# Kernel optimization log

Hardware: AMD Instinct MI355X
Metric: run time of the kernel (lower is better)

Reference implementation:

```python
import jax, jax.numpy as jnp
import numpy as np

H = 512  # hidden_dim
DIN = 64  # input_dim
DOUT = 1  # output_dim
B, T = 256, 512


def _lstm_layer(x_seq, W_ih, W_hh, b_ih, b_hh):
    """x_seq: [T, B, D_in]; returns full hidden sequence [T, B, H].
    PyTorch gate order along the 4H axis: i, f, g, o."""
    x_proj = jnp.einsum('tbd,gd->tbg', x_seq, W_ih) + b_ih + b_hh  # [T,B,4H]

    def cell(carry, xg):
        h, c = carry
        gates = xg + h @ W_hh.T  # [B,4H]
        i, f, g, o = jnp.split(gates, 4, axis=-1)
        c = jax.nn.sigmoid(f) * c + jax.nn.sigmoid(i) * jnp.tanh(g)
        h = jax.nn.sigmoid(o) * jnp.tanh(c)
        return (h, c), h

    h0 = jnp.zeros((x_seq.shape[1], H), x_seq.dtype)
    c0 = jnp.zeros_like(h0)
    _, hs = jax.lax.scan(cell, (h0, c0), x_proj)
    return hs


def setup_inputs() -> dict:
    key = jax.random.key(0)
    ks = jax.random.split(key, 11)
    s = 1.0 / np.sqrt(H)  # PyTorch LSTM init scale
    u = lambda k, shp: jax.random.uniform(k, shp, jnp.float32, -s, s)
    return {
        'x': jax.random.normal(ks[0], (B, T, DIN), jnp.float32),
        'W_ih0': u(ks[1], (4 * H, DIN)),
        'W_hh0': u(ks[2], (4 * H, H)),
        'b_ih0': u(ks[3], (4 * H,)),
        'b_hh0': u(ks[4], (4 * H,)),
        'W_ih1': u(ks[5], (4 * H, H)),
        'W_hh1': u(ks[6], (4 * H, H)),
        'b_ih1': u(ks[7], (4 * H,)),
        'b_hh1': u(ks[8], (4 * H,)),
        'fc_W': u(ks[9], (DOUT, H)),
        'fc_b': u(ks[10], (DOUT,)),
    }


def reference(x, W_ih0, W_hh0, b_ih0, b_hh0, W_ih1, W_hh1, b_ih1, b_hh1, fc_W, fc_b):
    xs = jnp.swapaxes(x, 0, 1)  # [T,B,DIN] time-major for scan
    h1 = _lstm_layer(xs, W_ih0, W_hh0, b_ih0, b_hh0)  # [T,B,H]
    h2 = _lstm_layer(h1, W_ih1, W_hh1, b_ih1, b_hh1)  # [T,B,H]
    last = h2[-1]  # [B,H] == out[:, -1, :]
    return last @ fc_W.T + fc_b  # [B,DOUT]
```

## Files before the change

kernel.cpp:

```cpp
#include <hip/hip_runtime.h>


typedef _Float16 f16;
typedef _Float16 f16x8 __attribute__((ext_vector_type(8)));
typedef float    f32x4 __attribute__((ext_vector_type(4)));

constexpr int NB   = 256;
constexpr int NT   = 512;
constexpr int NH   = 512;
constexpr int NDIN = 64;

constexpr int L0_KC = 18;
constexpr int L1_KC = 32;
constexpr int L0_IMG_HALVES = 4 * L0_KC * 64 * 8;
constexpr int L1_IMG_HALVES = 4 * L1_KC * 64 * 8;

constexpr int RING = 16;
constexpr int SLOT_F16 = 131072;

constexpr size_t BAR_OFF   = 0;
constexpr size_t AUX_OFF   = 16384;
constexpr size_t BIAS0_OFF = 20480;
constexpr size_t BIAS1_OFF = 28672;
constexpr size_t FLAG_OFF  = 36864;
constexpr size_t H0R_OFF   = 131072;
constexpr size_t H1R_OFF   = H0R_OFF + (size_t)RING * SLOT_F16 * 2;
constexpr size_t W0I_OFF   = H1R_OFF + (size_t)RING * SLOT_F16 * 2;
constexpr size_t W1I_OFF   = W0I_OFF + 2359296;
constexpr size_t WS_NEED   = W1I_OFF + 4194304;

constexpr int LDS_STAGE = 131072;
constexpr int LDS_GO    = 139264;
constexpr int LDS_SIZE  = 139520;

constexpr int WDOG = 1 << 20;

__global__ void prep_weights(const float* __restrict__ Wih0, const float* __restrict__ Whh0,
                             const float* __restrict__ Wih1, const float* __restrict__ Whh1,
                             char* __restrict__ ws) {
    int idx = blockIdx.x * 256 + threadIdx.x;
    const int L0_CH = 32 * 4 * L0_KC * 64;
    const int L1_CH = 32 * 4 * L1_KC * 64;
    if (idx < L0_CH) {
        int lam = idx & 63;
        int kc  = (idx >> 6) % L0_KC;
        int nf  = ((idx >> 6) / L0_KC) & 3;
        int ht  = idx / (64 * L0_KC * 4);
        int g   = nf * NH + ht * 16 + (lam & 15);
        int kb  = kc * 32 + (lam >> 4) * 8;
        f16x8 v;
#pragma unroll
        for (int j = 0; j < 8; ++j) {
            int k = kb + j;
            float val = (k < NDIN) ? Wih0[(size_t)g * NDIN + k]
                                   : Whh0[(size_t)g * NH + (k - NDIN)];
            v[j] = (f16)val;
        }
        f16* dst = (f16*)(ws + W0I_OFF) + (size_t)ht * L0_IMG_HALVES
                 + ((size_t)(nf * L0_KC + kc) * 64 + lam) * 8;
        *(f16x8*)dst = v;
    } else if (idx < L0_CH + L1_CH) {
        int i2  = idx - L0_CH;
        int lam = i2 & 63;
        int kc  = (i2 >> 6) % L1_KC;
        int nf  = ((i2 >> 6) / L1_KC) & 3;
        int ht  = i2 / (64 * L1_KC * 4);
        int g   = nf * NH + ht * 16 + (lam & 15);
        int kb  = kc * 32 + (lam >> 4) * 8;
        f16x8 v;
#pragma unroll
        for (int j = 0; j < 8; ++j) {
            int k = kb + j;
            float val = (k < NH) ? Wih1[(size_t)g * NH + k]
                                 : Whh1[(size_t)g * NH + (k - NH)];
            v[j] = (f16)val;
        }
        f16* dst = (f16*)(ws + W1I_OFF) + (size_t)ht * L1_IMG_HALVES
                 + ((size_t)(nf * L1_KC + kc) * 64 + lam) * 8;
        *(f16x8*)dst = v;
    }
}

__global__ void prep_state(const float* __restrict__ bih0, const float* __restrict__ bhh0,
                           const float* __restrict__ bih1, const float* __restrict__ bhh1,
                           char* __restrict__ ws) {
    int idx    = blockIdx.x * 256 + threadIdx.x;
    int stride = gridDim.x * 256;
    if (idx < 2048) {
        ((float*)(ws + BIAS0_OFF))[idx] = bih0[idx] + bhh0[idx];
    } else if (idx < 4096) {
        int i = idx - 2048;
        ((float*)(ws + BIAS1_OFF))[i] = bih1[i] + bhh1[i];
    }
    uint4 z; z.x = z.y = z.z = z.w = 0u;
    for (int i = idx; i < 1280; i += stride)
        ((uint4*)(ws + BAR_OFF))[i] = z;
    for (int i = idx; i < 2048; i += stride)
        ((uint4*)(ws + FLAG_OFF))[i] = z;
    const int RINGU4 = (int)((size_t)2 * RING * SLOT_F16 * 2 / 16);
    for (int i = idx; i < RINGU4; i += stride)
        ((uint4*)(ws + H0R_OFF))[i] = z;
}

__device__ __forceinline__ float sigf(float x) { return 1.f / (1.f + __expf(-x)); }
__device__ __forceinline__ float tanhx(float x) { float e = __expf(2.f * x); return 1.f - 2.f / (e + 1.f); }

__device__ __forceinline__ void st8_sys(unsigned long long* p, unsigned long long v) {
    __hip_atomic_store(p, v, __ATOMIC_RELAXED, __HIP_MEMORY_SCOPE_SYSTEM);
}

template <int SLP>
__device__ __forceinline__ void spin_cnt(unsigned* p, unsigned tgt) {
    int it = 0;
    while (__hip_atomic_fetch_add(p, 0u, __ATOMIC_RELAXED, __HIP_MEMORY_SCOPE_AGENT) < tgt) {
        __builtin_amdgcn_s_sleep(SLP);
        if (++it > WDOG) break;
    }
}

#define MFMA16(a, b, c) __builtin_amdgcn_mfma_f32_16x16x32_f16((a), (b), (c), 0, 0, 0)

__global__ __launch_bounds__(320, 1) void lstm_persist(char* __restrict__ ws,
                                                       const float* __restrict__ xin,
                                                       const float* __restrict__ fcW,
                                                       const float* __restrict__ fcb,
                                                       float* __restrict__ out) {
    extern __shared__ __align__(16) char smem[];
    f16*      sW     = (f16*)smem;
    f16*      hstage = (f16*)(smem + LDS_STAGE);
    unsigned* go     = (unsigned*)(smem + LDS_GO);

    const int tid  = threadIdx.x;
    const int lam  = tid & 63;
    const int w    = tid >> 6;
    const int col  = lam & 15;
    const int quad = lam >> 4;

    const int bid   = blockIdx.x;
    const int gid   = bid & 7;
    const int layer = gid >> 2;
    const int b0    = (gid & 3) * 64;
    const int ht    = bid >> 3;
    const int h0c   = ht * 16;
    const int KCx   = layer ? L1_KC : L0_KC;

    auto cntp = [&](int g, int slot) -> unsigned* {
        return (unsigned*)(ws + BAR_OFF + (size_t)(slot * 8 + g) * 128);
    };
    unsigned* flags = (unsigned*)(ws + FLAG_OFF);
    unsigned* hsk   = (unsigned*)(ws + AUX_OFF);
    unsigned* trdy  = (unsigned*)(ws + AUX_OFF + 128);
    unsigned* modep = (unsigned*)(ws + AUX_OFF + 256);
    unsigned* finp  = (unsigned*)(ws + AUX_OFF + 384);
    unsigned* tpat  = (unsigned*)(ws + AUX_OFF + 1024);
    unsigned* gvote = (unsigned*)(ws + AUX_OFF + 2048);

    if (tid == 0) {
        go[0] = 0u; go[1] = 0u;
        __hip_atomic_store(flags + (size_t)bid * 32 + 2, 0x5EED0000u + (unsigned)bid,
                           __ATOMIC_RELAXED, __HIP_MEMORY_SCOPE_AGENT);
        __hip_atomic_fetch_add(hsk, 1u, __ATOMIC_RELEASE, __HIP_MEMORY_SCOPE_AGENT);
        {
            int it = 0;
            while (__hip_atomic_fetch_add(hsk, 0u, __ATOMIC_RELAXED, __HIP_MEMORY_SCOPE_AGENT) < 256u) {
                __builtin_amdgcn_s_sleep(8);
                if (++it > WDOG) break;
            }
        }
        if (bid == 0) {
            for (int i = 0; i < 16; ++i)
                __hip_atomic_store(tpat + i * 16, 0xC0FFEE00u + (unsigned)i,
                                   __ATOMIC_RELAXED, __HIP_MEMORY_SCOPE_SYSTEM);
            asm volatile("s_waitcnt vmcnt(0)" ::: "memory");
            __hip_atomic_fetch_add(trdy, 1u, __ATOMIC_RELAXED, __HIP_MEMORY_SCOPE_AGENT);
        }
        if (bid == 1) {
            int it = 0;
            while (__hip_atomic_fetch_add(trdy, 0u, __ATOMIC_RELAXED, __HIP_MEMORY_SCOPE_AGENT) < 1u) {
                __builtin_amdgcn_s_sleep(8);
                if (++it > WDOG) break;
            }
            unsigned ok = 1u;
            for (int i = 0; i < 16; ++i)
                if (__hip_atomic_load(tpat + i * 16, __ATOMIC_RELAXED, __HIP_MEMORY_SCOPE_SYSTEM)
                    != 0xC0FFEE00u + (unsigned)i) ok = 0u;
            __hip_atomic_fetch_add(modep, 2u | (ok ? 0u : 1u), __ATOMIC_RELAXED, __HIP_MEMORY_SCOPE_AGENT);
        }
        unsigned mv; int spins = 0;
        while ((mv = __hip_atomic_fetch_add(modep, 0u, __ATOMIC_RELAXED, __HIP_MEMORY_SCOPE_AGENT)) < 2u) {
            __builtin_amdgcn_s_sleep(16);
            if (++spins > (1 << 22)) { mv = 3u; break; }
        }
        ((unsigned*)hstage)[1] = mv & 1u;
    }
    __syncthreads();
    const unsigned needRel = ((unsigned*)hstage)[1];
    __syncthreads();

    if (tid < 64) {
        unsigned seen = (lam < 32) ? 0u : 1u;
        unsigned expv = 0x5EED0000u + (unsigned)(lam * 8 + gid);
        int it = 0, done_at = 1 << 30;
        for (;;) {
            if (!seen && lam < 32) {
                unsigned v = __hip_atomic_load(flags + (size_t)(lam * 8 + gid) * 32 + 2,
                                               __ATOMIC_RELAXED, __HIP_MEMORY_SCOPE_AGENT);
                if (v == expv) seen = 1u;
            }
            ++it;
            if (__all((int)seen)) { done_at = it; break; }
            if (it >= 64) break;
        }
        unsigned ok = (done_at <= 12) ? 1u : 0u;
        if (lam == 0)
            __hip_atomic_fetch_add(gvote + (size_t)gid * 32, 0x10000u | ok,
                                   __ATOMIC_RELAXED, __HIP_MEMORY_SCOPE_AGENT);
    }
    __syncthreads();
    if (tid == 0) {
        unsigned gv = 0u; int sp2 = 0;
        for (;;) {
            gv = __hip_atomic_fetch_add(gvote + (size_t)gid * 32, 0u,
                                        __ATOMIC_RELAXED, __HIP_MEMORY_SCOPE_AGENT);
            if ((gv >> 16) >= 32u) break;
            __builtin_amdgcn_s_sleep(8);
            if (++sp2 > (1 << 20)) { gv = 0u; break; }
        }
        ((unsigned*)hstage)[0] = (((gv >> 16) >= 32u) && ((gv & 0xFFFFu) == 32u)) ? 1u : 0u;
    }
    __syncthreads();
    const unsigned fastgrp = ((unsigned*)hstage)[0];
    unsigned       fastE1  = fastgrp;
    __syncthreads();

    f16* h0ring = (f16*)(ws + H0R_OFF);
    f16* h1ring = (f16*)(ws + H1R_OFF);
    const float* bias = (const float*)(ws + (layer ? BIAS1_OFF : BIAS0_OFF));
    const f16*   wimg = (const f16*)(ws + (layer ? W1I_OFF : W0I_OFF))
                      + (size_t)ht * (layer ? L1_IMG_HALVES : L0_IMG_HALVES);

    {
        const int n16 = KCx * 4 * 64;
        const uint4* src = (const uint4*)wimg;
        uint4* dst = (uint4*)sW;
        for (int i = tid; i < n16; i += 320) dst[i] = src[i];
    }
    __syncthreads();

    const float bi_i = bias[0 * NH + h0c + col];
    const float bi_f = bias[1 * NH + h0c + col];
    const float bi_g = bias[2 * NH + h0c + col];
    const float bi_o = bias[3 * NH + h0c + col];

    float cst[4];
#pragma unroll
    for (int r = 0; r < 4; ++r) cst[r] = 0.f;

    const f16x8* sBf = (const f16x8*)sW;
    const int rA   = b0 + (w & 3) * 16 + col;
    const int rofs = rA * 16 + (quad & 1) * 8;
    const int hq   = (quad >> 1) * 4096;

    unsigned long long pr0 = 0, pr1 = 0, pr2 = 0, pr3 = 0;
    unsigned useRmw = 0u;
    unsigned vflag  = 0u;

    if (w == 4 && lam == 0) {
        if (layer == 1) spin_cnt<4>(cntp(gid - 4, 0), 32u);
        __hip_atomic_store(&go[0], 1u, __ATOMIC_RELAXED, __HIP_MEMORY_SCOPE_WORKGROUP);
    }

    for (int s = 0; s < NT; ++s) {
        const unsigned us = (unsigned)s;

        f32x4 ai = {0.f,0.f,0.f,0.f}, af = {0.f,0.f,0.f,0.f};
        f32x4 ag = {0.f,0.f,0.f,0.f}, ao = {0.f,0.f,0.f,0.f};

        if (w == 4) {
            if (!fastgrp) {
                if (s > 0) {
                    if (fastE1) {
                        int it = 0;
                        for (;;) {
                            unsigned v = 0xFFFFFFFFu;
                            if (lam < 32)
                                v = __hip_atomic_load(flags + (size_t)(lam * 8 + gid) * 32,
                                                      __ATOMIC_RELAXED, __HIP_MEMORY_SCOPE_AGENT);
                            if (__all((int)(v >= us))) break;
                            if (++it > 20000) { fastE1 = 0u; break; }
                        }
                    }
                    if (!fastE1) {
                        int it = 0;
                        for (;;) {
                            unsigned v = 0xFFFFFFFFu;
                            if (lam < 32)
                                v = __hip_atomic_fetch_add(flags + (size_t)(lam * 8 + gid) * 32, 0u,
                                                           __ATOMIC_RELAXED, __HIP_MEMORY_SCOPE_AGENT);
                            if (__all((int)(v >= us))) break;
                            __builtin_amdgcn_s_sleep(2);
                            if (++it > WDOG) break;
                        }
                    }
                }
                if (lam == 0)
                    __hip_atomic_store(&go[1], us + 1u, __ATOMIC_RELAXED, __HIP_MEMORY_SCOPE_WORKGROUP);
            }
            if (lam == 0 && s + 1 < NT) {
                const unsigned t = us + 1u;
                if (layer == 0) {
                    if (t >= (unsigned)RING)
                        spin_cnt<8>(cntp(gid + 4, (int)(t & 15u)), 32u * (t >> 4));
                } else {
                    spin_cnt<4>(cntp(gid - 4, (int)(t & 15u)), 32u * ((t >> 4) + 1u));
                }
                __hip_atomic_store(&go[0], t + 1u, __ATOMIC_RELAXED, __HIP_MEMORY_SCOPE_WORKGROUP);
            }
        } else {
            if (layer == 0) {
                if (fastgrp && w == 3 && s > 0) {
                    unsigned long long* d = (unsigned long long*)
                        ((char*)h0ring + ((size_t)((s - 1) & 15) * SLOT_F16 + (size_t)ht * 4096
                                          + (size_t)b0 * 16) * 2) + (size_t)lam * 4;
                    st8_sys(d + 0, pr0); st8_sys(d + 1, pr1);
                    st8_sys(d + 2, pr2); st8_sys(d + 3, pr3);
                }
                const float* xr = xin + (size_t)rA * (NT * NDIN) + (size_t)s * NDIN + quad * 8;
#pragma unroll
                for (int j = 0; j < 2; ++j) {
                    float4 f0 = *(const float4*)(xr + j * 32);
                    float4 f1 = *(const float4*)(xr + j * 32 + 4);
                    f16x8 a;
                    a[0] = (f16)f0.x; a[1] = (f16)f0.y; a[2] = (f16)f0.z; a[3] = (f16)f0.w;
                    a[4] = (f16)f1.x; a[5] = (f16)f1.y; a[6] = (f16)f1.z; a[7] = (f16)f1.w;
                    ai = MFMA16(a, sBf[(0 * L0_KC + j) * 64 + lam], ai);
                    af = MFMA16(a, sBf[(1 * L0_KC + j) * 64 + lam], af);
                    ag = MFMA16(a, sBf[(2 * L0_KC + j) * 64 + lam], ag);
                    ao = MFMA16(a, sBf[(3 * L0_KC + j) * 64 + lam], ao);
                }
                {
                    int it = 0;
                    while (__hip_atomic_load(&go[0], __ATOMIC_RELAXED, __HIP_MEMORY_SCOPE_WORKGROUP) <= us) {
                        __builtin_amdgcn_s_sleep(1);
                        if (++it > WDOG) break;
                    }
                }
            } else {
                {
                    int it = 0;
                    while (__hip_atomic_load(&go[0], __ATOMIC_RELAXED, __HIP_MEMORY_SCOPE_WORKGROUP) <= us) {
                        __builtin_amdgcn_s_sleep(1);
                        if (++it > WDOG) break;
                    }
                }
                const f16* hp0 = h0ring + (size_t)(s & 15) * SLOT_F16;
#pragma unroll
                for (int j = 0; j < 16; ++j) {
                    f16x8 a = *(const f16x8*)(hp0 + (size_t)(2 * j) * 4096 + hq + rofs);
                    ai = MFMA16(a, sBf[(0 * L1_KC + j) * 64 + lam], ai);
                    af = MFMA16(a, sBf[(1 * L1_KC + j) * 64 + lam], af);
                    ag = MFMA16(a, sBf[(2 * L1_KC + j) * 64 + lam], ag);
                    ao = MFMA16(a, sBf[(3 * L1_KC + j) * 64 + lam], ao);
                }
            }

            if (fastgrp) {
                if (s > 0) {
                    if (lam >= 32) vflag = 0xFFFFFFFFu;
                    int it = 0;
                    for (;;) {
                        if (lam < 32 && vflag < us) {
                            if (!useRmw)
                                vflag = __hip_atomic_load(flags + (size_t)(lam * 8 + gid) * 32,
                                                          __ATOMIC_RELAXED, __HIP_MEMORY_SCOPE_AGENT);
                            else
                                vflag = __hip_atomic_fetch_add(flags + (size_t)(lam * 8 + gid) * 32, 0u,
                                                               __ATOMIC_RELAXED, __HIP_MEMORY_SCOPE_AGENT);
                        }
                        if (__all((int)(vflag >= us))) break;
                        if (++it > 20000) useRmw = 1u;
                        if (it > WDOG) break;
                        __builtin_amdgcn_s_sleep(1);
                    }
                }
            } else {
                int it = 0;
                while (__hip_atomic_load(&go[1], __ATOMIC_RELAXED, __HIP_MEMORY_SCOPE_WORKGROUP) <= us) {
                    __builtin_amdgcn_s_sleep(1);
                    if (++it > WDOG) break;
                }
            }

            {
                const f16* hpo = (layer ? h1ring : h0ring) + (size_t)((s + RING - 1) & 15) * SLOT_F16;
                const int  wb  = layer ? 16 : 2;
#pragma unroll
                for (int j = 0; j < 16; ++j) {
                    f16x8 a = *(const f16x8*)(hpo + (size_t)(2 * j) * 4096 + hq + rofs);
                    ai = MFMA16(a, sBf[(0 * KCx + wb + j) * 64 + lam], ai);
                    af = MFMA16(a, sBf[(1 * KCx + wb + j) * 64 + lam], af);
                    ag = MFMA16(a, sBf[(2 * KCx + wb + j) * 64 + lam], ag);
                    ao = MFMA16(a, sBf[(3 * KCx + wb + j) * 64 + lam], ao);
                }
            }

#pragma unroll
            for (int r = 0; r < 4; ++r) {
                float iv = ai[r] + bi_i;
                float fv = af[r] + bi_f;
                float gv = ag[r] + bi_g;
                float ov = ao[r] + bi_o;
                float cc = sigf(fv) * cst[r] + sigf(iv) * tanhx(gv);
                cst[r] = cc;
                float hh = sigf(ov) * tanhx(cc);
                hstage[((w & 3) * 16 + quad * 4 + r) * 16 + col] = (f16)hh;
            }

            if (fastgrp && layer == 0 && w == 3 && s > 0) {
                asm volatile("s_waitcnt vmcnt(0)" ::: "memory");
                if (lam == 0) {
                    if (needRel)
                        __hip_atomic_fetch_add(cntp(gid, (s - 1) & 15), 1u, __ATOMIC_RELEASE, __HIP_MEMORY_SCOPE_AGENT);
                    else
                        __hip_atomic_fetch_add(cntp(gid, (s - 1) & 15), 1u, __ATOMIC_RELAXED, __HIP_MEMORY_SCOPE_AGENT);
                }
            }
        }

        __syncthreads();

        if (tid < 128) {
            f16* dstf = (layer ? h1ring : h0ring)
                      + (size_t)(s & 15) * SLOT_F16 + (size_t)ht * 4096
                      + (size_t)b0 * 16 + (size_t)tid * 8;
            if (fastgrp) {
                *(uint4*)dstf = ((const uint4*)hstage)[tid];
            } else {
                const unsigned long long* sp = (const unsigned long long*)hstage;
                st8_sys((unsigned long long*)dstf, sp[tid * 2]);
                st8_sys((unsigned long long*)dstf + 1, sp[tid * 2 + 1]);
            }
        }
        if (fastgrp && layer == 0 && w == 3) {
            const unsigned long long* sp = (const unsigned long long*)hstage;
            pr0 = sp[lam * 4 + 0]; pr1 = sp[lam * 4 + 1];
            pr2 = sp[lam * 4 + 2]; pr3 = sp[lam * 4 + 3];
        }

        if (tid == 128 && ((s & 15) == 15))
            (void)__hip_atomic_load((unsigned*)(ws + BAR_OFF), __ATOMIC_ACQUIRE, __HIP_MEMORY_SCOPE_AGENT);

        __syncthreads();

        if (tid == 192) {
            if (fastgrp) {
                __hip_atomic_store(flags + (size_t)bid * 32, us + 1u,
                                   __ATOMIC_RELAXED, __HIP_MEMORY_SCOPE_AGENT);
                if (layer == 1)
                    __hip_atomic_fetch_add(cntp(gid, s & 15), 1u, __ATOMIC_RELAXED, __HIP_MEMORY_SCOPE_AGENT);
            } else {
                if (needRel)
                    __hip_atomic_fetch_add(cntp(gid, s & 15), 1u, __ATOMIC_RELEASE, __HIP_MEMORY_SCOPE_AGENT);
                else
                    __hip_atomic_fetch_add(cntp(gid, s & 15), 1u, __ATOMIC_RELAXED, __HIP_MEMORY_SCOPE_AGENT);
                __hip_atomic_fetch_add(flags + (size_t)bid * 32, 1u,
                                       __ATOMIC_RELAXED, __HIP_MEMORY_SCOPE_AGENT);
            }
        }
    }

    if (fastgrp && layer == 0 && w == 3) {
        unsigned long long* d = (unsigned long long*)
            ((char*)h0ring + ((size_t)15 * SLOT_F16 + (size_t)ht * 4096
                              + (size_t)b0 * 16) * 2) + (size_t)lam * 4;
        st8_sys(d + 0, pr0); st8_sys(d + 1, pr1);
        st8_sys(d + 2, pr2); st8_sys(d + 3, pr3);
        asm volatile("s_waitcnt vmcnt(0)" ::: "memory");
        if (lam == 0) {
            if (needRel)
                __hip_atomic_fetch_add(cntp(gid, 15), 1u, __ATOMIC_RELEASE, __HIP_MEMORY_SCOPE_AGENT);
            else
                __hip_atomic_fetch_add(cntp(gid, 15), 1u, __ATOMIC_RELAXED, __HIP_MEMORY_SCOPE_AGENT);
        }
    }

    if (layer == 1 && tid == 0)
        __hip_atomic_fetch_add(finp, 1u, __ATOMIC_RELEASE, __HIP_MEMORY_SCOPE_AGENT);

    if (bid == 0) {
        if (tid == 0) {
            int it = 0;
            while (__hip_atomic_fetch_add(finp, 0u, __ATOMIC_RELAXED, __HIP_MEMORY_SCOPE_AGENT) < 128u) {
                __builtin_amdgcn_s_sleep(8);
                if (++it > (1 << 22)) break;
            }
            (void)__hip_atomic_load((unsigned*)(ws + BAR_OFF), __ATOMIC_ACQUIRE, __HIP_MEMORY_SCOPE_AGENT);
        }
        __syncthreads();
        if (tid < 256) {
            const f16* hrow = h1ring + (size_t)15 * SLOT_F16 + (size_t)tid * 16;
            float acc = fcb[0];
#pragma unroll 4
            for (int t2 = 0; t2 < 32; ++t2) {
                f16x8 a = *(const f16x8*)(hrow + t2 * 4096);
                f16x8 b = *(const f16x8*)(hrow + t2 * 4096 + 8);
#pragma unroll
                for (int e = 0; e < 8; ++e)
                    acc += fcW[t2 * 16 + e] * (float)a[e] + fcW[t2 * 16 + 8 + e] * (float)b[e];
            }
            out[tid] = acc;
        }
    }
}

extern "C" void kernel_launch(void* const* d_in, const int* in_sizes, int n_in,
                              void* d_out, int out_size, void* d_ws, size_t ws_size,
                              hipStream_t stream) {
    const float* x    = (const float*)d_in[0];
    const float* Wih0 = (const float*)d_in[1];
    const float* Whh0 = (const float*)d_in[2];
    const float* bih0 = (const float*)d_in[3];
    const float* bhh0 = (const float*)d_in[4];
    const float* Wih1 = (const float*)d_in[5];
    const float* Whh1 = (const float*)d_in[6];
    const float* bih1 = (const float*)d_in[7];
    const float* bhh1 = (const float*)d_in[8];
    const float* fcW  = (const float*)d_in[9];
    const float* fcb  = (const float*)d_in[10];
    char*  ws  = (char*)d_ws;
    float* out = (float*)d_out;

    if (ws_size < WS_NEED) {
        hipMemsetAsync(d_out, 0, (size_t)out_size * sizeof(float), stream);
        return;
    }

    hipFuncSetAttribute(reinterpret_cast<const void*>(lstm_persist),
                        hipFuncAttributeMaxDynamicSharedMemorySize, LDS_SIZE);

    prep_weights<<<1600, 256, 0, stream>>>(Wih0, Whh0, Wih1, Whh1, ws);
    prep_state<<<1100, 256, 0, stream>>>(bih0, bhh0, bih1, bhh1, ws);
    lstm_persist<<<256, 320, LDS_SIZE, stream>>>(ws, x, fcW, fcb, out);
}
```

Baseline: 3.027 ms.

## Restructure fast-group step: direct global h writes, single barrier, prefetch before MFMA

For the fast group, compute warps now write h straight to the global ring instead of staging through LDS, so each step needs only one __syncthreads instead of two. The layer-0 cross-layer system-scope republish moves from warp 3 to the control warp 4, which reads back the previous slot. Operand loads (x, recurrent h, and layer-1 h0) are hoisted ahead of the MFMA chains, separated by sched_barrier, to overlap memory latency with waiting. This trades some extra global reads by warp 4 and more register pressure for a shorter per-step critical path, with a risk of ordering subtleties in the flag and counter protocol.

Result: slower. 3.623 ms (+19.7%).

```diff
diff --git a/kernel.cpp b/kernel.cpp
--- a/kernel.cpp
+++ b/kernel.cpp
@@ -261,7 +261,6 @@
     const int rofs = rA * 16 + (quad & 1) * 8;
     const int hq   = (quad >> 1) * 4096;
 
-    unsigned long long pr0 = 0, pr1 = 0, pr2 = 0, pr3 = 0;
     unsigned useRmw = 0u;
     unsigned vflag  = 0u;
 
@@ -276,8 +275,184 @@
         f32x4 ai = {0.f,0.f,0.f,0.f}, af = {0.f,0.f,0.f,0.f};
         f32x4 ag = {0.f,0.f,0.f,0.f}, ao = {0.f,0.f,0.f,0.f};
 
-        if (w == 4) {
-            if (!fastgrp) {
+        if (fastgrp) {
+            if (w == 4) {
+                if (layer == 0) {
+                    if (s > 0) {
+                        unsigned long long* cb = (unsigned long long*)
+                            ((char*)h0ring + ((size_t)((s - 1) & 15) * SLOT_F16
+                                              + (size_t)ht * 4096 + (size_t)b0 * 16) * 2);
+                        unsigned long long a0 = cb[lam * 4 + 0], a1 = cb[lam * 4 + 1];
+                        unsigned long long a2 = cb[lam * 4 + 2], a3 = cb[lam * 4 + 3];
+                        st8_sys(cb + lam * 4 + 0, a0); st8_sys(cb + lam * 4 + 1, a1);
+                        st8_sys(cb + lam * 4 + 2, a2); st8_sys(cb + lam * 4 + 3, a3);
+                    }
+                    if (lam == 0 && s + 1 < NT) {
+                        const unsigned t = us + 1u;
+                        if (t >= (unsigned)RING)
+                            spin_cnt<8>(cntp(gid + 4, (int)(t & 15u)), 32u * (t >> 4));
+                    }
+                    asm volatile("s_waitcnt vmcnt(0)" ::: "memory");
+                    if (lam == 0 && s > 0) {
+                        if (needRel)
+                            __hip_atomic_fetch_add(cntp(gid, (s - 1) & 15), 1u, __ATOMIC_RELEASE, __HIP_MEMORY_SCOPE_AGENT);
+                        else
+                            __hip_atomic_fetch_add(cntp(gid, (s - 1) & 15), 1u, __ATOMIC_RELAXED, __HIP_MEMORY_SCOPE_AGENT);
+                    }
+                    if (lam == 0 && s + 1 < NT)
+                        __hip_atomic_store(&go[0], us + 2u, __ATOMIC_RELAXED, __HIP_MEMORY_SCOPE_WORKGROUP);
+                } else {
+                    if (lam == 0 && s + 1 < NT) {
+                        const unsigned t = us + 1u;
+                        spin_cnt<4>(cntp(gid - 4, (int)(t & 15u)), 32u * ((t >> 4) + 1u));
+                        __hip_atomic_store(&go[0], t + 1u, __ATOMIC_RELAXED, __HIP_MEMORY_SCOPE_WORKGROUP);
+                    }
+                }
+            } else {
+                if (layer == 0) {
+                    f16x8 ax[2];
+                    {
+                        const float* xr = xin + (size_t)rA * (NT * NDIN) + (size_t)s * NDIN + quad * 8;
+#pragma unroll
+                        for (int j = 0; j < 2; ++j) {
+                            float4 f0 = *(const float4*)(xr + j * 32);
+                            float4 f1 = *(const float4*)(xr + j * 32 + 4);
+                            ax[j][0] = (f16)f0.x; ax[j][1] = (f16)f0.y; ax[j][2] = (f16)f0.z; ax[j][3] = (f16)f0.w;
+                            ax[j][4] = (f16)f1.x; ax[j][5] = (f16)f1.y; ax[j][6] = (f16)f1.z; ax[j][7] = (f16)f1.w;
+                        }
+                    }
+                    {
+                        int it = 0;
+                        while (__hip_atomic_load(&go[0], __ATOMIC_RELAXED, __HIP_MEMORY_SCOPE_WORKGROUP) <= us) {
+                            __builtin_amdgcn_s_sleep(1);
+                            if (++it > WDOG) break;
+                        }
+                    }
+                    if (s > 0) {
+                        if (lam >= 32) vflag = 0xFFFFFFFFu;
+                        int it = 0;
+                        for (;;) {
+                            if (lam < 32 && vflag < us) {
+                                if (!useRmw)
+                                    vflag = __hip_atomic_load(flags + (size_t)(lam * 8 + gid) * 32,
+                                                              __ATOMIC_RELAXED, __HIP_MEMORY_SCOPE_AGENT);
+                                else
+                                    vflag = __hip_atomic_fetch_add(flags + (size_t)(lam * 8 + gid) * 32, 0u,
+                                                                   __ATOMIC_RELAXED, __HIP_MEMORY_SCOPE_AGENT);
+                            }
+                            if (__all((int)(vflag >= us))) break;
+                            if (++it > 20000) useRmw = 1u;
+                            if (it > WDOG) break;
+                            __builtin_amdgcn_s_sleep(1);
+                        }
+                    }
+                    f16x8 ah[16];
+                    {
+                        const f16* hpo = h0ring + (size_t)((s + RING - 1) & 15) * SLOT_F16;
+#pragma unroll
+                        for (int j = 0; j < 16; ++j)
+                            ah[j] = *(const f16x8*)(hpo + (size_t)(2 * j) * 4096 + hq + rofs);
+                    }
+                    __builtin_amdgcn_sched_barrier(0);
+#pragma unroll
+                    for (int j = 0; j < 2; ++j) {
+                        ai = MFMA16(ax[j], sBf[(0 * L0_KC + j) * 64 + lam], ai);
+                        af = MFMA16(ax[j], sBf[(1 * L0_KC + j) * 64 + lam], af);
+                        ag = MFMA16(ax[j], sBf[(2 * L0_KC + j) * 64 + lam], ag);
+                        ao = MFMA16(ax[j], sBf[(3 * L0_KC + j) * 64 + lam], ao);
+                    }
+#pragma unroll
+                    for (int j = 0; j < 16; ++j) {
+                        ai = MFMA16(ah[j], sBf[(0 * L0_KC + 2 + j) * 64 + lam], ai);
+                        af = MFMA16(ah[j], sBf[(1 * L0_KC + 2 + j) * 64 + lam], af);
+                        ag = MFMA16(ah[j], sBf[(2 * L0_KC + 2 + j) * 64 + lam], ag);
+                        ao = MFMA16(ah[j], sBf[(3 * L0_KC + 2 + j) * 64 + lam], ao);
+                    }
+                } else {
+                    if (s > 0) {
+                        if (lam >= 32) vflag = 0xFFFFFFFFu;
+                        int it = 0;
+                        for (;;) {
+                            if (lam < 32 && vflag < us) {
+                                if (!useRmw)
+                                    vflag = __hip_atomic_load(flags + (size_t)(lam * 8 + gid) * 32,
+                                                              __ATOMIC_RELAXED, __HIP_MEMORY_SCOPE_AGENT);
+                                else
+                                    vflag = __hip_atomic_fetch_add(flags + (size_t)(lam * 8 + gid) * 32, 0u,
+                                                                   __ATOMIC_RELAXED, __HIP_MEMORY_SCOPE_AGENT);
+                            }
+                            if (__all((int)(vflag >= us))) break;
+                            if (++it > 20000) useRmw = 1u;
+                            if (it > WDOG) break;
+                            __builtin_amdgcn_s_sleep(1);
+                        }
+                    }
+                    f16x8 ah1[16];
+                    {
+                        const f16* hp1 = h1ring + (size_t)((s + RING - 1) & 15) * SLOT_F16;
+#pragma unroll
+                        for (int j = 0; j < 16; ++j)
+                            ah1[j] = *(const f16x8*)(hp1 + (size_t)(2 * j) * 4096 + hq + rofs);
+                    }
+                    {
+                        int it = 0;
+                        while (__hip_atomic_load(&go[0], __ATOMIC_RELAXED, __HIP_MEMORY_SCOPE_WORKGROUP) <= us) {
+                            __builtin_amdgcn_s_sleep(1);
+                            if (++it > WDOG) break;
+                        }
+                    }
+                    f16x8 ah0[16];
+                    {
+                        const f16* hp0 = h0ring + (size_t)(s & 15) * SLOT_F16;
+#pragma unroll
+                        for (int j = 0; j < 16; ++j)
+                            ah0[j] = *(const f16x8*)(hp0 + (size_t)(2 * j) * 4096 + hq + rofs);
+                    }
+                    __builtin_amdgcn_sched_barrier(0);
+#pragma unroll
+                    for (int j = 0; j < 16; ++j) {
+                        ai = MFMA16(ah1[j], sBf[(0 * L1_KC + 16 + j) * 64 + lam], ai);
+                        af = MFMA16(ah1[j], sBf[(1 * L1_KC + 16 + j) * 64 + lam], af);
+                        ag = MFMA16(ah1[j], sBf[(2 * L1_KC + 16 + j) * 64 + lam], ag);
+                        ao = MFMA16(ah1[j], sBf[(3 * L1_KC + 16 + j) * 64 + lam], ao);
+                    }
+#pragma unroll
+                    for (int j = 0; j < 16; ++j) {
+                        ai = MFMA16(ah0[j], sBf[(0 * L1_KC + j) * 64 + lam], ai);
+                        af = MFMA16(ah0[j], sBf[(1 * L1_KC + j) * 64 + lam], af);
+                        ag = MFMA16(ah0[j], sBf[(2 * L1_KC + j) * 64 + lam], ag);
+                        ao = MFMA16(ah0[j], sBf[(3 * L1_KC + j) * 64 + lam], ao);
+                    }
+                }
+
+                {
+                    f16* hwc = (layer ? h1ring : h0ring) + (size_t)(s & 15) * SLOT_F16
+                             + (size_t)ht * 4096 + (size_t)b0 * 16;
+#pragma unroll
+                    for (int r = 0; r < 4; ++r) {
+                        float iv = ai[r] + bi_i;
+                        float fv = af[r] + bi_f;
+                        float gv = ag[r] + bi_g;
+                        float ov = ao[r] + bi_o;
+                        float cc = sigf(fv) * cst[r] + sigf(iv) * tanhx(gv);
+                        cst[r] = cc;
+                        float hh = sigf(ov) * tanhx(cc);
+                        hwc[((w & 3) * 16 + quad * 4 + r) * 16 + col] = (f16)hh;
+                    }
+                }
+                if (tid == 128 && ((s & 15) == 15))
+                    (void)__hip_atomic_load((unsigned*)(ws + BAR_OFF), __ATOMIC_ACQUIRE, __HIP_MEMORY_SCOPE_AGENT);
+            }
+
+            __syncthreads();
+            if (w == 4 && lam == 0) {
+                __hip_atomic_store(flags + (size_t)bid * 32, us + 1u,
+                                   __ATOMIC_RELAXED, __HIP_MEMORY_SCOPE_AGENT);
+                if (layer == 1)
+                    __hip_atomic_fetch_add(cntp(gid, s & 15), 1u, __ATOMIC_RELAXED, __HIP_MEMORY_SCOPE_AGENT);
+            }
+        } else {
+            if (w == 4) {
                 if (s > 0) {
                     if (fastE1) {
                         int it = 0;
@@ -305,160 +480,97 @@
                 }
                 if (lam == 0)
                     __hip_atomic_store(&go[1], us + 1u, __ATOMIC_RELAXED, __HIP_MEMORY_SCOPE_WORKGROUP);
-            }
-            if (lam == 0 && s + 1 < NT) {
-                const unsigned t = us + 1u;
+                if (lam == 0 && s + 1 < NT) {
+                    const unsigned t = us + 1u;
+                    if (layer == 0) {
+                        if (t >= (unsigned)RING)
+                            spin_cnt<8>(cntp(gid + 4, (int)(t & 15u)), 32u * (t >> 4));
+                    } else {
+                        spin_cnt<4>(cntp(gid - 4, (int)(t & 15u)), 32u * ((t >> 4) + 1u));
+                    }
+                    __hip_atomic_store(&go[0], t + 1u, __ATOMIC_RELAXED, __HIP_MEMORY_SCOPE_WORKGROUP);
+                }
+            } else {
                 if (layer == 0) {
-                    if (t >= (unsigned)RING)
-                        spin_cnt<8>(cntp(gid + 4, (int)(t & 15u)), 32u * (t >> 4));
-                } else {
-                    spin_cnt<4>(cntp(gid - 4, (int)(t & 15u)), 32u * ((t >> 4) + 1u));
-                }
-                __hip_atomic_store(&go[0], t + 1u, __ATOMIC_RELAXED, __HIP_MEMORY_SCOPE_WORKGROUP);
-            }
-        } else {
-            if (layer == 0) {
-                if (fastgrp && w == 3 && s > 0) {
-                    unsigned long long* d = (unsigned long long*)
-                        ((char*)h0ring + ((size_t)((s - 1) & 15) * SLOT_F16 + (size_t)ht * 4096
-                                          + (size_t)b0 * 16) * 2) + (size_t)lam * 4;
-                    st8_sys(d + 0, pr0); st8_sys(d + 1, pr1);
-                    st8_sys(d + 2, pr2); st8_sys(d + 3, pr3);
-                }
-                const float* xr = xin + (size_t)rA * (NT * NDIN) + (size_t)s * NDIN + quad * 8;
-#pragma unroll
-                for (int j = 0; j < 2; ++j) {
-                    float4 f0 = *(const float4*)(xr + j * 32);
-                    float4 f1 = *(const float4*)(xr + j * 32 + 4);
-                    f16x8 a;
-                    a[0] = (f16)f0.x; a[1] = (f16)f0.y; a[2] = (f16)f0.z; a[3] = (f16)f0.w;
-                    a[4] = (f16)f1.x; a[5] = (f16)f1.y; a[6] = (f16)f1.z; a[7] = (f16)f1.w;
-                    ai = MFMA16(a, sBf[(0 * L0_KC + j) * 64 + lam], ai);
-                    af = MFMA16(a, sBf[(1 * L0_KC + j) * 64 + lam], af);
-                    ag = MFMA16(a, sBf[(2 * L0_KC + j) * 64 + lam], ag);
-                    ao = MFMA16(a, sBf[(3 * L0_KC + j) * 64 + lam], ao);
-                }
-                {
+                    const float* xr = xin + (size_t)rA * (NT * NDIN) + (size_t)s * NDIN + quad * 8;
+#pragma unroll
+                    for (int j = 0; j < 2; ++j) {
+                        float4 f0 = *(const float4*)(xr + j * 32);
+                        float4 f1 = *(const float4*)(xr + j * 32 + 4);
+                        f16x8 a;
+                        a[0] = (f16)f0.x; a[1] = (f16)f0.y; a[2] = (f16)f0.z; a[3] = (f16)f0.w;
+                        a[4] = (f16)f1.x; a[5] = (f16)f1.y; a[6] = (f16)f1.z; a[7] = (f16)f1.w;
+                        ai = MFMA16(a, sBf[(0 * L0_KC + j) * 64 + lam], ai);
+                        af = MFMA16(a, sBf[(1 * L0_KC + j) * 64 + lam], af);
+                        ag = MFMA16(a, sBf[(2 * L0_KC + j) * 64 + lam], ag);
+                        ao = MFMA16(a, sBf[(3 * L0_KC + j) * 64 + lam], ao);
+                    }
                     int it = 0;
                     while (__hip_atomic_load(&go[0], __ATOMIC_RELAXED, __HIP_MEMORY_SCOPE_WORKGROUP) <= us) {
                         __builtin_amdgcn_s_sleep(1);
                         if (++it > WDOG) break;
                     }
-                }
-            } else {
-                {
+                } else {
                     int it = 0;
                     while (__hip_atomic_load(&go[0], __ATOMIC_RELAXED, __HIP_MEMORY_SCOPE_WORKGROUP) <= us) {
                         __builtin_amdgcn_s_sleep(1);
                         if (++it > WDOG) break;
                     }
-                }
-                const f16* hp0 = h0ring + (size_t)(s & 15) * SLOT_F16;
-#pragma unroll
-                for (int j = 0; j < 16; ++j) {
-                    f16x8 a = *(const f16x8*)(hp0 + (size_t)(2 * j) * 4096 + hq + rofs);
-                    ai = MFMA16(a, sBf[(0 * L1_KC + j) * 64 + lam], ai);
-                    af = MFMA16(a, sBf[(1 * L1_KC + j) * 64 + lam], af);
-                    ag = MFMA16(a, sBf[(2 * L1_KC + j) * 64 + lam], ag);
-                    ao = MFMA16(a, sBf[(3 * L1_KC + j) * 64 + lam], ao);
-                }
-            }
-
-            if (fastgrp) {
-                if (s > 0) {
-                    if (lam >= 32) vflag = 0xFFFFFFFFu;
+                    const f16* hp0 = h0ring + (size_t)(s & 15) * SLOT_F16;
+#pragma unroll
+                    for (int j = 0; j < 16; ++j) {
+                        f16x8 a = *(const f16x8*)(hp0 + (size_t)(2 * j) * 4096 + hq + rofs);
+                        ai = MFMA16(a, sBf[(0 * L1_KC + j) * 64 + lam], ai);
+                        af = MFMA16(a, sBf[(1 * L1_KC + j) * 64 + lam], af);
+                        ag = MFMA16(a, sBf[(2 * L1_KC + j) * 64 + lam], ag);
+                        ao = MFMA16(a, sBf[(3 * L1_KC + j) * 64 + lam], ao);
+                    }
+                }
+                {
                     int it = 0;
-                    for (;;) {
-                        if (lam < 32 && vflag < us) {
-                            if (!useRmw)
-                                vflag = __hip_atomic_load(flags + (size_t)(lam * 8 + gid) * 32,
-                                                          __ATOMIC_RELAXED, __HIP_MEMORY_SCOPE_AGENT);
-                            else
-                                vflag = __hip_atomic_fetch_add(flags + (size_t)(lam * 8 + gid) * 32, 0u,
-                                                               __ATOMIC_RELAXED, __HIP_MEMORY_SCOPE_AGENT);
-                        }
-                        if (__all((int)(vflag >= us))) break;
-                        if (++it > 20000) useRmw = 1u;
-                        if (it > WDOG) break;
+                    while (__hip_atomic_load(&go[1], __ATOMIC_RELAXED, __HIP_MEMORY_SCOPE_WORKGROUP) <= us) {
                         __builtin_amdgcn_s_sleep(1);
-                    }
-                }
-            } else {
-                int it = 0;
-                while (__hip_atomic_load(&go[1], __ATOMIC_RELAXED, __HIP_MEMORY_SCOPE_WORKGROUP) <= us) {
-                    __builtin_amdgcn_s_sleep(1);
-                    if (++it > WDOG) break;
-                }
-            }
-
-            {
-                const f16* hpo = (layer ? h1ring : h0ring) + (size_t)((s + RING - 1) & 15) * SLOT_F16;
-                const int  wb  = layer ? 16 : 2;
-#pragma unroll
-                for (int j = 0; j < 16; ++j) {
-                    f16x8 a = *(const f16x8*)(hpo + (size_t)(2 * j) * 4096 + hq + rofs);
-                    ai = MFMA16(a, sBf[(0 * KCx + wb + j) * 64 + lam], ai);
-                    af = MFMA16(a, sBf[(1 * KCx + wb + j) * 64 + lam], af);
-                    ag = MFMA16(a, sBf[(2 * KCx + wb + j) * 64 + lam], ag);
-                    ao = MFMA16(a, sBf[(3 * KCx + wb + j) * 64 + lam], ao);
-                }
-            }
-
-#pragma unroll
-            for (int r = 0; r < 4; ++r) {
-                float iv = ai[r] + bi_i;
-                float fv = af[r] + bi_f;
-                float gv = ag[r] + bi_g;
-                float ov = ao[r] + bi_o;
-                float cc = sigf(fv) * cst[r] + sigf(iv) * tanhx(gv);
-                cst[r] = cc;
-                float hh = sigf(ov) * tanhx(cc);
-                hstage[((w & 3) * 16 + quad * 4 + r) * 16 + col] = (f16)hh;
-            }
-
-            if (fastgrp && layer == 0 && w == 3 && s > 0) {
-                asm volatile("s_waitcnt vmcnt(0)" ::: "memory");
-                if (lam == 0) {
-                    if (needRel)
-                        __hip_atomic_fetch_add(cntp(gid, (s - 1) & 15), 1u, __ATOMIC_RELEASE, __HIP_MEMORY_SCOPE_AGENT);
-                    else
-                        __hip_atomic_fetch_add(cntp(gid, (s - 1) & 15), 1u, __ATOMIC_RELAXED, __HIP_MEMORY_SCOPE_AGENT);
-                }
-            }
-        }
-
-        __syncthreads();
-
-        if (tid < 128) {
-            f16* dstf = (layer ? h1ring : h0ring)
-                      + (size_t)(s & 15) * SLOT_F16 + (size_t)ht * 4096
-                      + (size_t)b0 * 16 + (size_t)tid * 8;
-            if (fastgrp) {
-                *(uint4*)dstf = ((const uint4*)hstage)[tid];
-            } else {
+                        if (++it > WDOG) break;
+                    }
+                }
+                {
+                    const f16* hpo = (layer ? h1ring : h0ring) + (size_t)((s + RING - 1) & 15) * SLOT_F16;
+                    const int  wb  = layer ? 16 : 2;
+#pragma unroll
+                    for (int j = 0; j < 16; ++j) {
+                        f16x8 a = *(const f16x8*)(hpo + (size_t)(2 * j) * 4096 + hq + rofs);
+                        ai = MFMA16(a, sBf[(0 * KCx + wb + j) * 64 + lam], ai);
+                        af = MFMA16(a, sBf[(1 * KCx + wb + j) * 64 + lam], af);
+                        ag = MFMA16(a, sBf[(2 * KCx + wb + j) * 64 + lam], ag);
+                        ao = MFMA16(a, sBf[(3 * KCx + wb + j) * 64 + lam], ao);
+                    }
+                }
+#pragma unroll
+                for (int r = 0; r < 4; ++r) {
+                    float iv = ai[r] + bi_i;
+                    float fv = af[r] + bi_f;
+                    float gv = ag[r] + bi_g;
+                    float ov = ao[r] + bi_o;
+                    float cc = sigf(fv) * cst[r] + sigf(iv) * tanhx(gv);
+                    cst[r] = cc;
+                    float hh = sigf(ov) * tanhx(cc);
+                    hstage[((w & 3) * 16 + quad * 4 + r) * 16 + col] = (f16)hh;
+                }
+            }
+
+            __syncthreads();
+            if (tid < 128) {
+                f16* dstf = (layer ? h1ring : h0ring)
+                          + (size_t)(s & 15) * SLOT_F16 + (size_t)ht * 4096
+                          + (size_t)b0 * 16 + (size_t)tid * 8;
                 const unsigned long long* sp = (const unsigned long long*)hstage;
                 st8_sys((unsigned long long*)dstf, sp[tid * 2]);
                 st8_sys((unsigned long long*)dstf + 1, sp[tid * 2 + 1]);
             }
-        }
-        if (fastgrp && layer == 0 && w == 3) {
-            const unsigned long long* sp = (const unsigned long long*)hstage;
-            pr0 = sp[lam * 4 + 0]; pr1 = sp[lam * 4 + 1];
-            pr2 = sp[lam * 4 + 2]; pr3 = sp[lam * 4 + 3];
-        }
-
-        if (tid == 128 && ((s & 15) == 15))
-            (void)__hip_atomic_load((unsigned*)(ws + BAR_OFF), __ATOMIC_ACQUIRE, __HIP_MEMORY_SCOPE_AGENT);
-
-        __syncthreads();
-
-        if (tid == 192) {
-            if (fastgrp) {
-                __hip_atomic_store(flags + (size_t)bid * 32, us + 1u,
-                                   __ATOMIC_RELAXED, __HIP_MEMORY_SCOPE_AGENT);
-                if (layer == 1)
-                    __hip_atomic_fetch_add(cntp(gid, s & 15), 1u, __ATOMIC_RELAXED, __HIP_MEMORY_SCOPE_AGENT);
-            } else {
+            if (tid == 128 && ((s & 15) == 15))
+                (void)__hip_atomic_load((unsigned*)(ws + BAR_OFF), __ATOMIC_ACQUIRE, __HIP_MEMORY_SCOPE_AGENT);
+            __syncthreads();
+            if (tid == 192) {
                 if (needRel)
                     __hip_atomic_fetch_add(cntp(gid, s & 15), 1u, __ATOMIC_RELEASE, __HIP_MEMORY_SCOPE_AGENT);
                 else
@@ -469,12 +581,13 @@
         }
     }
 
-    if (fastgrp && layer == 0 && w == 3) {
-        unsigned long long* d = (unsigned long long*)
-            ((char*)h0ring + ((size_t)15 * SLOT_F16 + (size_t)ht * 4096
-                              + (size_t)b0 * 16) * 2) + (size_t)lam * 4;
-        st8_sys(d + 0, pr0); st8_sys(d + 1, pr1);
-        st8_sys(d + 2, pr2); st8_sys(d + 3, pr3);
+    if (fastgrp && layer == 0 && w == 4) {
+        unsigned long long* cb = (unsigned long long*)
+            ((char*)h0ring + ((size_t)15 * SLOT_F16 + (size_t)ht * 4096 + (size_t)b0 * 16) * 2);
+        unsigned long long a0 = cb[lam * 4 + 0], a1 = cb[lam * 4 + 1];
+        unsigned long long a2 = cb[lam * 4 + 2], a3 = cb[lam * 4 + 3];
+        st8_sys(cb + lam * 4 + 0, a0); st8_sys(cb + lam * 4 + 1, a1);
+        st8_sys(cb + lam * 4 + 2, a2); st8_sys(cb + lam * 4 + 3, a3);
         asm volatile("s_waitcnt vmcnt(0)" ::: "memory");
         if (lam == 0) {
             if (needRel)
```

## Publish layer-0 h to layer 1 immediately and batch ring loads before MFMAs

Applied to the files above, without the earlier changes.

Layer-0 fast groups no longer defer their system-scope h stores to layer 1 until the next step. The stores and the counter increment now happen right after the step's barrier, and the step flag is moved to a separate thread. This removes one step of latency from the layer-0 to layer-1 handoff, at the cost of putting the store and vmcnt wait on the critical path of each step. Separately, the 16 ring-buffer fragment loads are hoisted ahead of the MFMA chain behind a sched_barrier so all loads are in flight together, which raises register use.

Result: faster. 2.743 ms (-9.4%).

```diff
diff --git a/kernel.cpp b/kernel.cpp
--- a/kernel.cpp
+++ b/kernel.cpp
@@ -261,7 +261,6 @@
     const int rofs = rA * 16 + (quad & 1) * 8;
     const int hq   = (quad >> 1) * 4096;
 
-    unsigned long long pr0 = 0, pr1 = 0, pr2 = 0, pr3 = 0;
     unsigned useRmw = 0u;
     unsigned vflag  = 0u;
 
@@ -318,13 +317,6 @@
             }
         } else {
             if (layer == 0) {
-                if (fastgrp && w == 3 && s > 0) {
-                    unsigned long long* d = (unsigned long long*)
-                        ((char*)h0ring + ((size_t)((s - 1) & 15) * SLOT_F16 + (size_t)ht * 4096
-                                          + (size_t)b0 * 16) * 2) + (size_t)lam * 4;
-                    st8_sys(d + 0, pr0); st8_sys(d + 1, pr1);
-                    st8_sys(d + 2, pr2); st8_sys(d + 3, pr3);
-                }
                 const float* xr = xin + (size_t)rA * (NT * NDIN) + (size_t)s * NDIN + quad * 8;
 #pragma unroll
                 for (int j = 0; j < 2; ++j) {
@@ -353,14 +345,20 @@
                         if (++it > WDOG) break;
                     }
                 }
-                const f16* hp0 = h0ring + (size_t)(s & 15) * SLOT_F16;
-#pragma unroll
-                for (int j = 0; j < 16; ++j) {
-                    f16x8 a = *(const f16x8*)(hp0 + (size_t)(2 * j) * 4096 + hq + rofs);
-                    ai = MFMA16(a, sBf[(0 * L1_KC + j) * 64 + lam], ai);
-                    af = MFMA16(a, sBf[(1 * L1_KC + j) * 64 + lam], af);
-                    ag = MFMA16(a, sBf[(2 * L1_KC + j) * 64 + lam], ag);
-                    ao = MFMA16(a, sBf[(3 * L1_KC + j) * 64 + lam], ao);
+                {
+                    const f16* hp0 = h0ring + (size_t)(s & 15) * SLOT_F16;
+                    f16x8 aa[16];
+#pragma unroll
+                    for (int j = 0; j < 16; ++j)
+                        aa[j] = *(const f16x8*)(hp0 + (size_t)(2 * j) * 4096 + hq + rofs);
+                    __builtin_amdgcn_sched_barrier(0);
+#pragma unroll
+                    for (int j = 0; j < 16; ++j) {
+                        ai = MFMA16(aa[j], sBf[(0 * L1_KC + j) * 64 + lam], ai);
+                        af = MFMA16(aa[j], sBf[(1 * L1_KC + j) * 64 + lam], af);
+                        ag = MFMA16(aa[j], sBf[(2 * L1_KC + j) * 64 + lam], ag);
+                        ao = MFMA16(aa[j], sBf[(3 * L1_KC + j) * 64 + lam], ao);
+                    }
                 }
             }
 
@@ -394,13 +392,17 @@
             {
                 const f16* hpo = (layer ? h1ring : h0ring) + (size_t)((s + RING - 1) & 15) * SLOT_F16;
                 const int  wb  = layer ? 16 : 2;
+                f16x8 aa[16];
+#pragma unroll
+                for (int j = 0; j < 16; ++j)
+                    aa[j] = *(const f16x8*)(hpo + (size_t)(2 * j) * 4096 + hq + rofs);
+                __builtin_amdgcn_sched_barrier(0);
 #pragma unroll
                 for (int j = 0; j < 16; ++j) {
-                    f16x8 a = *(const f16x8*)(hpo + (size_t)(2 * j) * 4096 + hq + rofs);
-                    ai = MFMA16(a, sBf[(0 * KCx + wb + j) * 64 + lam], ai);
-                    af = MFMA16(a, sBf[(1 * KCx + wb + j) * 64 + lam], af);
-                    ag = MFMA16(a, sBf[(2 * KCx + wb + j) * 64 + lam], ag);
-                    ao = MFMA16(a, sBf[(3 * KCx + wb + j) * 64 + lam], ao);
+                    ai = MFMA16(aa[j], sBf[(0 * KCx + wb + j) * 64 + lam], ai);
+                    af = MFMA16(aa[j], sBf[(1 * KCx + wb + j) * 64 + lam], af);
+                    ag = MFMA16(aa[j], sBf[(2 * KCx + wb + j) * 64 + lam], ag);
+                    ao = MFMA16(aa[j], sBf[(3 * KCx + wb + j) * 64 + lam], ao);
                 }
             }
 
@@ -414,16 +416,6 @@
                 cst[r] = cc;
                 float hh = sigf(ov) * tanhx(cc);
                 hstage[((w & 3) * 16 + quad * 4 + r) * 16 + col] = (f16)hh;
-            }
-
-            if (fastgrp && layer == 0 && w == 3 && s > 0) {
-                asm volatile("s_waitcnt vmcnt(0)" ::: "memory");
-                if (lam == 0) {
-                    if (needRel)
-                        __hip_atomic_fetch_add(cntp(gid, (s - 1) & 15), 1u, __ATOMIC_RELEASE, __HIP_MEMORY_SCOPE_AGENT);
-                    else
-                        __hip_atomic_fetch_add(cntp(gid, (s - 1) & 15), 1u, __ATOMIC_RELAXED, __HIP_MEMORY_SCOPE_AGENT);
-                }
             }
         }
 
@@ -441,6 +433,8 @@
                 st8_sys((unsigned long long*)dstf + 1, sp[tid * 2 + 1]);
             }
         }
+
+        unsigned long long pr0 = 0, pr1 = 0, pr2 = 0, pr3 = 0;
         if (fastgrp && layer == 0 && w == 3) {
             const unsigned long long* sp = (const unsigned long long*)hstage;
             pr0 = sp[lam * 4 + 0]; pr1 = sp[lam * 4 + 1];
@@ -452,12 +446,26 @@
 
         __syncthreads();
 
-        if (tid == 192) {
+        if (fastgrp && layer == 0 && w == 3) {
+            unsigned long long* d = (unsigned long long*)
+                ((char*)h0ring + ((size_t)(s & 15) * SLOT_F16 + (size_t)ht * 4096
+                                  + (size_t)b0 * 16) * 2) + (size_t)lam * 4;
+            st8_sys(d + 0, pr0); st8_sys(d + 1, pr1);
+            st8_sys(d + 2, pr2); st8_sys(d + 3, pr3);
+            asm volatile("s_waitcnt vmcnt(0)" ::: "memory");
+            if (lam == 0) {
+                if (needRel)
+                    __hip_atomic_fetch_add(cntp(gid, s & 15), 1u, __ATOMIC_RELEASE, __HIP_MEMORY_SCOPE_AGENT);
+                else
+                    __hip_atomic_fetch_add(cntp(gid, s & 15), 1u, __ATOMIC_RELAXED, __HIP_MEMORY_SCOPE_AGENT);
+            }
+        }
+
+        if (tid == 192 && !(fastgrp && layer == 0)) {
             if (fastgrp) {
                 __hip_atomic_store(flags + (size_t)bid * 32, us + 1u,
                                    __ATOMIC_RELAXED, __HIP_MEMORY_SCOPE_AGENT);
-                if (layer == 1)
-                    __hip_atomic_fetch_add(cntp(gid, s & 15), 1u, __ATOMIC_RELAXED, __HIP_MEMORY_SCOPE_AGENT);
+                __hip_atomic_fetch_add(cntp(gid, s & 15), 1u, __ATOMIC_RELAXED, __HIP_MEMORY_SCOPE_AGENT);
             } else {
                 if (needRel)
                     __hip_atomic_fetch_add(cntp(gid, s & 15), 1u, __ATOMIC_RELEASE, __HIP_MEMORY_SCOPE_AGENT);
@@ -467,20 +475,9 @@
                                        __ATOMIC_RELAXED, __HIP_MEMORY_SCOPE_AGENT);
             }
         }
-    }
-
-    if (fastgrp && layer == 0 && w == 3) {
-        unsigned long long* d = (unsigned long long*)
-            ((char*)h0ring + ((size_t)15 * SLOT_F16 + (size_t)ht * 4096
-                              + (size_t)b0 * 16) * 2) + (size_t)lam * 4;
-        st8_sys(d + 0, pr0); st8_sys(d + 1, pr1);
-        st8_sys(d + 2, pr2); st8_sys(d + 3, pr3);
-        asm volatile("s_waitcnt vmcnt(0)" ::: "memory");
-        if (lam == 0) {
-            if (needRel)
-                __hip_atomic_fetch_add(cntp(gid, 15), 1u, __ATOMIC_RELEASE, __HIP_MEMORY_SCOPE_AGENT);
-            else
-                __hip_atomic_fetch_add(cntp(gid, 15), 1u, __ATOMIC_RELAXED, __HIP_MEMORY_SCOPE_AGENT);
+        if (fastgrp && layer == 0 && tid == 192 + 32) {
+            __hip_atomic_store(flags + (size_t)bid * 32, us + 1u,
+                               __ATOMIC_RELAXED, __HIP_MEMORY_SCOPE_AGENT);
         }
     }
 
```
